# Kernel optimization log

Hardware: AMD Instinct MI355X
Metric: run time of the kernel (lower is better)

Reference implementation:

```python
import jax, jax.numpy as jnp
import numpy as np

N, E, G = 50000, 800000, 500
F_IN, H_DIM, L, NH, HD, OUT = 74, 256, 4, 8, 32, 1
SLOPE, EPS = 0.2, 1e-5


def setup_inputs() -> dict:
    key = jax.random.key(0)
    ks = jax.random.split(key, 24)
    rn = lambda k, s, sc: jax.random.normal(k, s, jnp.float32) * sc
    inp = {
        "x": jax.random.normal(ks[0], (N, F_IN), jnp.float32),
        "edge_index": jax.random.randint(ks[1], (2, E), 0, N),
        "batch": jnp.sort(jax.random.randint(ks[2], (N,), 0, G)),
        "in_w": rn(ks[3], (F_IN, H_DIM), 1.0 / np.sqrt(F_IN)),
        "in_b": jnp.zeros((H_DIM,), jnp.float32),
        "wl": rn(ks[4], (L, H_DIM, H_DIM), 1.0 / np.sqrt(H_DIM)),
        "wl_b": jnp.zeros((L, H_DIM), jnp.float32),
        "wr": rn(ks[5], (L, H_DIM, H_DIM), 1.0 / np.sqrt(H_DIM)),
        "wr_b": jnp.zeros((L, H_DIM), jnp.float32),
        "att": rn(ks[6], (L, NH, HD), 1.0 / np.sqrt(HD)),
        "gat_b": jnp.zeros((L, H_DIM), jnp.float32),
        "ln_g": jnp.ones((L, H_DIM), jnp.float32),
        "ln_b": jnp.zeros((L, H_DIM), jnp.float32),
        "out_w": rn(ks[7], (H_DIM, H_DIM), 1.0 / np.sqrt(H_DIM)),
        "out_b": jnp.zeros((H_DIM,), jnp.float32),
        "p1_w": rn(ks[8], (H_DIM, H_DIM // 2), 1.0 / np.sqrt(H_DIM)),
        "p1_b": jnp.zeros((H_DIM // 2,), jnp.float32),
        "bn1_g": jnp.ones((H_DIM // 2,), jnp.float32),
        "bn1_b": jnp.zeros((H_DIM // 2,), jnp.float32),
        "p2_w": rn(ks[9], (H_DIM // 2, H_DIM // 4), 1.0 / np.sqrt(H_DIM // 2)),
        "p2_b": jnp.zeros((H_DIM // 4,), jnp.float32),
        "bn2_g": jnp.ones((H_DIM // 4,), jnp.float32),
        "bn2_b": jnp.zeros((H_DIM // 4,), jnp.float32),
        "p3_w": rn(ks[10], (H_DIM // 4, OUT), 1.0 / np.sqrt(H_DIM // 4)),
        "p3_b": jnp.zeros((OUT,), jnp.float32),
    }
    return inp


def _layer_norm(x, g, b):
    m = x.mean(-1, keepdims=True)
    v = ((x - m) ** 2).mean(-1, keepdims=True)
    return (x - m) * jax.lax.rsqrt(v + EPS) * g + b


def _batch_norm(x, g, b):
    m = x.mean(0)
    v = ((x - m) ** 2).mean(0)
    return (x - m) * jax.lax.rsqrt(v + EPS) * g + b


def _gatv2(h, src, dst, wl, wl_b, wr, wr_b, att, bias, n):
    xl = (h @ wl + wl_b).reshape(n, NH, HD)  # source transform
    xr = (h @ wr + wr_b).reshape(n, NH, HD)  # target transform
    e = jax.nn.leaky_relu(xl[src] + xr[dst], SLOPE)      # [E, H, D]
    score = jnp.einsum('ehd,hd->eh', e, att)             # [E, H]
    smax = jax.ops.segment_max(score, dst, num_segments=n)
    num = jnp.exp(score - smax[dst])
    den = jax.ops.segment_sum(num, dst, num_segments=n)
    alpha = num / (den[dst] + 1e-16)                     # segment softmax per dst
    out = jax.ops.segment_sum(xl[src] * alpha[:, :, None], dst, num_segments=n)
    return out.reshape(n, NH * HD) + bias


def reference(x, edge_index, batch, in_w, in_b, wl, wl_b, wr, wr_b, att, gat_b,
              ln_g, ln_b, out_w, out_b, p1_w, p1_b, bn1_g, bn1_b,
              p2_w, p2_b, bn2_g, bn2_b, p3_w, p3_b):
    n = x.shape[0]
    loops = jnp.arange(n)
    src = jnp.concatenate([edge_index[0], loops])  # add self-loops (PyG default)
    dst = jnp.concatenate([edge_index[1], loops])
    h = x @ in_w + in_b
    for i in range(L):
        res = h
        g = _gatv2(h, src, dst, wl[i], wl_b[i], wr[i], wr_b[i], att[i], gat_b[i], n)
        if i > 0:
            g = g + res
        h = jax.nn.relu(_layer_norm(g, ln_g[i], ln_b[i]))
    h = h @ out_w + out_b
    cnt = jax.ops.segment_sum(jnp.ones((n,), h.dtype), batch, num_segments=G)
    gr = jax.ops.segment_sum(h, batch, num_segments=G) / jnp.maximum(cnt, 1.0)[:, None]
    z = jax.nn.relu(_batch_norm(gr @ p1_w + p1_b, bn1_g, bn1_b))
    z = jax.nn.relu(_batch_norm(z @ p2_w + p2_b, bn2_g, bn2_b))
    return z @ p3_w + p3_b
```

## Files before the change

kernel.cpp:

```cpp
#include <hip/hip_runtime.h>
#include <hip/hip_bf16.h>

#define F_IN   74
#define KPAD   96
#define HDIM   256
#define NHEAD  8
#define HEADD  32
#define NLAYER 4
#define SLOPE  0.2f
#define EPSN   1e-5f
#define LOG2E  1.44269504088896f

typedef __attribute__((ext_vector_type(8))) short bf16x8;
typedef __attribute__((ext_vector_type(4))) float f32x4;
typedef __attribute__((ext_vector_type(2))) float f32x2;

__device__ __forceinline__ float bf2f(unsigned short u){
  union { unsigned int i; float f; } x; x.i = ((unsigned int)u) << 16; return x.f;
}
__device__ __forceinline__ unsigned short f2bf(float f){
  union { float f; unsigned int i; } x; x.f = f;
  unsigned int u = x.i;
  return (unsigned short)((u + 0x7FFFu + ((u >> 16) & 1u)) >> 16);
}
__device__ __forceinline__ f32x2 bfpair(unsigned int u){
  union { unsigned int i; float f; } lo, hi;
  lo.i = u << 16; hi.i = u & 0xffff0000u;
  return (f32x2){lo.f, hi.f};
}
__device__ __forceinline__ float hw_exp2(float p){
  float r;
  asm volatile("v_exp_f32 %0, %1" : "=v"(r) : "v"(p));
  return r;
}
__device__ __forceinline__ float dpp_sum8(float p){
  int t;
  t = __builtin_amdgcn_update_dpp(0, __float_as_int(p), 0xB1, 0xF, 0xF, true);
  p += __int_as_float(t);
  t = __builtin_amdgcn_update_dpp(0, __float_as_int(p), 0x4E, 0xF, 0xF, true);
  p += __int_as_float(t);
  t = __builtin_amdgcn_update_dpp(0, __float_as_int(p), 0x141, 0xF, 0xF, true);
  p += __int_as_float(t);
  return p;
}
__device__ __forceinline__ float dpp_sum16(float p){
  int t;
  p = dpp_sum8(p);
  t = __builtin_amdgcn_update_dpp(0, __float_as_int(p), 0x140, 0xF, 0xF, true);
  p += __int_as_float(t);
  return p;
}

#define GLOAD16(g, s) __builtin_amdgcn_global_load_lds( \
  (const __attribute__((address_space(1))) void*)(g), \
  (__attribute__((address_space(3))) void*)(s), 16, 0, 0)

__global__ void k_hist(const int* __restrict__ dst, int* __restrict__ deg, int e){
  int i = blockIdx.x * 256 + threadIdx.x;
  if (i < e) atomicAdd(&deg[dst[i]], 1);
}

__global__ __launch_bounds__(256) void k_scan1(const int* __restrict__ deg,
    int* __restrict__ rowp, int* __restrict__ bsum, int n){
  __shared__ int wsum[4];
  const int tid = threadIdx.x, lane = tid & 63, wid = tid >> 6;
  const int i = blockIdx.x * 256 + tid;
  int v = (i < n) ? (deg[i] + 1) : 0;
  int xv = v;
  #pragma unroll
  for (int off = 1; off < 64; off <<= 1){
    int t = __shfl_up(xv, off);
    if (lane >= off) xv += t;
  }
  if (lane == 63) wsum[wid] = xv;
  __syncthreads();
  int woff = 0, total = 0;
  #pragma unroll
  for (int w = 0; w < 4; ++w){
    int s = wsum[w];
    total += s;
    if (w < wid) woff += s;
  }
  if (i < n) rowp[i] = woff + xv - v;
  if (tid == 0) bsum[blockIdx.x] = total;
}
__global__ __launch_bounds__(256) void k_scan2(const int* __restrict__ bsum,
    int* __restrict__ boff, int nb){
  __shared__ int wsum[4];
  const int tid = threadIdx.x, lane = tid & 63, wid = tid >> 6;
  int v = (tid < nb) ? bsum[tid] : 0;
  int xv = v;
  #pragma unroll
  for (int off = 1; off < 64; off <<= 1){
    int t = __shfl_up(xv, off);
    if (lane >= off) xv += t;
  }
  if (lane == 63) wsum[wid] = xv;
  __syncthreads();
  int woff = 0, total = 0;
  #pragma unroll
  for (int w = 0; w < 4; ++w){
    int s = wsum[w];
    total += s;
    if (w < wid) woff += s;
  }
  if (tid <= nb) boff[tid] = woff + xv - v;
  if (tid == 0) boff[nb] = total;
}
__global__ void k_scan3(int* __restrict__ rowp, int* __restrict__ cur,
                        const int* __restrict__ boff, int n, int nb){
  int i = blockIdx.x * 256 + threadIdx.x;
  if (i < n){
    int v = rowp[i] + boff[blockIdx.x];
    rowp[i] = v;
    cur[i] = v;
  }
  if (i == 0) rowp[n] = boff[nb];
}

__global__ void k_fill2(const int* __restrict__ src, const int* __restrict__ dst,
                        int* __restrict__ cur, unsigned int* __restrict__ csr,
                        int e, int n){
  int i = blockIdx.x * 256 + threadIdx.x;
  if (i < e){
    int p = atomicAdd(&cur[dst[i]], 1);
    csr[p] = ((unsigned int)src[i]) << 10;
  } else if (i < e + n){
    int v = i - e;
    int p = atomicAdd(&cur[v], 1);
    csr[p] = ((unsigned int)v) << 10;
  }
}

__global__ __launch_bounds__(256) void k_prep(
    const float* __restrict__ wl, const float* __restrict__ wr,
    const float* __restrict__ out_w, const float* __restrict__ in_w,
    const float* __restrict__ wl_b, const float* __restrict__ wr_b,
    const float* __restrict__ x,
    unsigned short* __restrict__ WtLR, unsigned short* __restrict__ WtO,
    unsigned short* __restrict__ WtI, float* __restrict__ bconc,
    unsigned short* __restrict__ xb, int n)
{
  const int b = blockIdx.x;
  const int tid = threadIdx.x;
  if (b < 576){
    __shared__ float tile[32][33];
    const float* Wm;
    unsigned short* Wo;
    int rem, colbase;
    if (b < 512){
      const int matset = b >> 8;
      const int mat = (b >> 6) & 3;
      rem = b & 63;
      const float* srcw = matset ? wr : wl;
      Wm = srcw + (size_t)mat * HDIM * HDIM;
      Wo = WtLR + (size_t)mat * 512 * HDIM;
      colbase = matset * 256;
    } else {
      rem = b - 512;
      Wm = out_w; Wo = WtO; colbase = 0;
    }
    const int c0 = (rem & 7) * 32, r0 = (rem >> 3) * 32;
    const int tx = tid & 31, ty = tid >> 5;
    #pragma unroll
    for (int i = 0; i < 32; i += 8)
      tile[ty + i][tx] = Wm[(size_t)(r0 + ty + i) * HDIM + c0 + tx];
    __syncthreads();
    #pragma unroll
    for (int i = 0; i < 32; i += 8){
      const int col = colbase + c0 + ty + i;
      const int k   = r0 + tx;
      const int cb = col >> 4, ks = k >> 5;
      const int lf = (col & 15) | (((k >> 3) & 3) << 4);
      Wo[((size_t)(cb * 8 + ks) * 64 + lf) * 8 + (k & 7)] = f2bf(tile[tx][ty + i]);
    }
  } else if (b < 672){
    int idx = (b - 576) * 256 + tid;
    int c = idx / KPAD, k = idx - c * KPAD;
    float v = (k < F_IN) ? in_w[(size_t)k * HDIM + c] : 0.f;
    WtI[idx] = f2bf(v);
  } else if (b < 680){
    int i = (b - 672) * 256 + tid;
    if (i < NLAYER * 512){
      int layer = i >> 9, c = i & 511;
      bconc[i] = (c < 256) ? wl_b[layer * 256 + c] : wr_b[layer * 256 + (c - 256)];
    }
  } else {
    int idx = (b - 680) * 256 + tid;
    if (idx < n * KPAD){
      int row = idx / KPAD, k = idx - row * KPAD;
      float v = (k < F_IN) ? x[(size_t)row * F_IN + k] : 0.f;
      xb[idx] = f2bf(v);
    }
  }
}

__global__ __launch_bounds__(256) void k_inproj_mfma(
    const unsigned short* __restrict__ xb, const unsigned short* __restrict__ Wt,
    const float* __restrict__ bias, unsigned short* __restrict__ C, int M)
{
  const int l = threadIdx.x & 63;
  const int w = threadIdx.x >> 6;
  const int wm = w >> 1, wn = w & 1;
  const int row0 = blockIdx.x * 128;
  const int col0 = blockIdx.y * 128;

  f32x4 acc[4][4];
  #pragma unroll
  for (int i = 0; i < 4; ++i)
    #pragma unroll
    for (int j = 0; j < 4; ++j) acc[i][j] = (f32x4){0.f, 0.f, 0.f, 0.f};

  #pragma unroll
  for (int kk = 0; kk < 3; ++kk){
    const int kof = kk * 32 + (l >> 4) * 8;
    bf16x8 af[4], bfr[4];
    #pragma unroll
    for (int mi = 0; mi < 4; ++mi){
      int row = row0 + wm * 64 + mi * 16 + (l & 15);
      if (row > M - 1) row = M - 1;
      af[mi] = *(const bf16x8*)(xb + (size_t)row * KPAD + kof);
    }
    #pragma unroll
    for (int ni = 0; ni < 4; ++ni){
      const int col = col0 + wn * 64 + ni * 16 + (l & 15);
      bfr[ni] = *(const bf16x8*)(Wt + (size_t)col * KPAD + kof);
    }
    #pragma unroll
    for (int mi = 0; mi < 4; ++mi)
      #pragma unroll
      for (int ni = 0; ni < 4; ++ni)
        acc[mi][ni] = __builtin_amdgcn_mfma_f32_16x16x32_bf16(
            af[mi], bfr[ni], acc[mi][ni], 0, 0, 0);
  }

  #pragma unroll
  for (int mi = 0; mi < 4; ++mi){
    #pragma unroll
    for (int ni = 0; ni < 4; ++ni){
      const int col = col0 + wn * 64 + ni * 16 + (l & 15);
      const float bv = bias[col];
      #pragma unroll
      for (int r = 0; r < 4; ++r){
        const int row = row0 + wm * 64 + mi * 16 + (l >> 4) * 4 + r;
        if (row < M) C[(size_t)row * HDIM + col] = f2bf(acc[mi][ni][r] + bv);
      }
    }
  }
}

__global__ __launch_bounds__(256) void k_gemm_mfma(
    const unsigned short* __restrict__ A, const unsigned short* __restrict__ Wt,
    const float* __restrict__ bias, unsigned short* __restrict__ C, int M, int ldc)
{
  __shared__ unsigned short As[2][128 * 64];
  const int tid = threadIdx.x;
  const int l   = tid & 63;
  const int w   = tid >> 6;
  const int wm  = w >> 1, wn = w & 1;
  const int row0 = blockIdx.x * 128;
  const int col0 = blockIdx.y * 128;

  const int srow   = l >> 3;
  const int schunk = l & 7;

  f32x4 acc[4][4];
  #pragma unroll
  for (int i = 0; i < 4; ++i)
    #pragma unroll
    for (int j = 0; j < 4; ++j) acc[i][j] = (f32x4){0.f, 0.f, 0.f, 0.f};

  auto stageA = [&](int buf, int k0){
    #pragma unroll
    for (int i = 0; i < 4; ++i){
      const int rloc = w * 32 + i * 8 + srow;
      const int sw   = (schunk ^ (rloc & 7)) * 16;
      int ra = row0 + rloc; if (ra > M - 1) ra = M - 1;
      const char* srcA = (const char*)(A + (size_t)ra * HDIM + k0) + sw;
      GLOAD16(srcA, &As[buf][(w * 32 + i * 8) * 64]);
    }
  };

  const unsigned short* Bf = Wt + ((size_t)(col0 / 16 + wn * 4) * 8 * 64 + l) * 8;

  stageA(0, 0);
  asm volatile("s_waitcnt vmcnt(0)" ::: "memory");
  __builtin_amdgcn_s_barrier();
  int buf = 0;
  #pragma unroll
  for (int t = 0; t < 4; ++t){
    bf16x8 bfr[2][4];
    #pragma unroll
    for (int kk = 0; kk < 2; ++kk)
      #pragma unroll
      for (int ni = 0; ni < 4; ++ni)
        bfr[kk][ni] = *(const bf16x8*)(Bf + ((size_t)ni * 8 + (t * 2 + kk)) * 64 * 8);
    if (t < 3) stageA(buf ^ 1, (t + 1) * 64);
    #pragma unroll
    for (int kk = 0; kk < 2; ++kk){
      bf16x8 af[4];
      #pragma unroll
      for (int mi = 0; mi < 4; ++mi){
        const int row = wm * 64 + mi * 16 + (l & 15);
        const int tt  = (kk * 4 + (l >> 4)) ^ (row & 7);
        af[mi] = *(const bf16x8*)((const char*)&As[buf][0] + row * 128 + tt * 16);
      }
      #pragma unroll
      for (int mi = 0; mi < 4; ++mi)
        #pragma unroll
        for (int ni = 0; ni < 4; ++ni)
          acc[mi][ni] = __builtin_amdgcn_mfma_f32_16x16x32_bf16(
              af[mi], bfr[kk][ni], acc[mi][ni], 0, 0, 0);
    }
    if (t < 3){
      asm volatile("s_waitcnt vmcnt(0)" ::: "memory");
      __builtin_amdgcn_s_barrier();
      buf ^= 1;
    }
  }

  #pragma unroll
  for (int mi = 0; mi < 4; ++mi){
    #pragma unroll
    for (int ni = 0; ni < 4; ++ni){
      const int col = col0 + wn * 64 + ni * 16 + (l & 15);
      const float bv = bias[col];
      #pragma unroll
      for (int r = 0; r < 4; ++r){
        const int row = row0 + wm * 64 + mi * 16 + (l >> 4) * 4 + r;
        if (row < M) C[(size_t)row * ldc + col] = f2bf(acc[mi][ni][r] + bv);
      }
    }
  }
}

__global__ __launch_bounds__(256) void k_gat(
    const unsigned short* __restrict__ xlr,
    const int* __restrict__ rp, const unsigned int* __restrict__ csr,
    const float* __restrict__ att, const float* __restrict__ gb,
    const float* __restrict__ lg, const float* __restrict__ lb,
    const unsigned short* __restrict__ hold, unsigned short* __restrict__ hnew,
    int n, int use_res)
{
  const int node = blockIdx.x * 4 + (threadIdx.x >> 6);
  if (node >= n) return;
  const int lane = threadIdx.x & 63;
  const int elem = lane << 2;
  const int head = lane >> 3;
  float4 attv = *(const float4*)(att + head * HEADD + (elem & 31));
  const f32x2 av01 = {attv.x * LOG2E, attv.y * LOG2E};
  const f32x2 av23 = {attv.z * LOG2E, attv.w * LOG2E};
  uint2 ur = *(const uint2*)(xlr + (size_t)node * 512 + 256 + elem);
  const f32x2 r01 = bfpair(ur.x), r23 = bfpair(ur.y);

  const unsigned int ebyte = (unsigned int)(elem << 1);
  const char* xb8 = (const char*)xlr;

  f32x2 a01 = {0.f, 0.f}, a23 = {0.f, 0.f};
  float l = 0.f;

  auto edgeq = [&](uint2 uu, f32x2& x01, f32x2& x23)->float{
    x01 = bfpair(uu.x); x23 = bfpair(uu.y);
    f32x2 t01 = x01 + r01, t23 = x23 + r23;
    f32x2 m01 = __builtin_elementwise_max(t01, t01 * SLOPE);
    f32x2 m23 = __builtin_elementwise_max(t23, t23 * SLOPE);
    f32x2 d = m01 * av01 + m23 * av23;
    float p = dpp_sum8(d.x + d.y);
    return hw_exp2(p);
  };

  const int e0 = rp[node], e1 = rp[node + 1];
  int e = e0;
  for (; e + 4 <= e1; e += 4){
    unsigned int o0 = csr[e] | ebyte, o1 = csr[e + 1] | ebyte;
    unsigned int o2 = csr[e + 2] | ebyte, o3 = csr[e + 3] | ebyte;
    uint2 u0 = *(const uint2*)(xb8 + o0);
    uint2 u1 = *(const uint2*)(xb8 + o1);
    uint2 u2 = *(const uint2*)(xb8 + o2);
    uint2 u3 = *(const uint2*)(xb8 + o3);
    f32x2 x01, x23;
    float q0 = edgeq(u0, x01, x23);
    a01 += q0 * x01; a23 += q0 * x23;
    float q1 = edgeq(u1, x01, x23);
    a01 += q1 * x01; a23 += q1 * x23;
    float q2 = edgeq(u2, x01, x23);
    a01 += q2 * x01; a23 += q2 * x23;
    float q3 = edgeq(u3, x01, x23);
    a01 += q3 * x01; a23 += q3 * x23;
    l += (q0 + q1) + (q2 + q3);
  }
  for (; e < e1; ++e){
    unsigned int o = csr[e] | ebyte;
    uint2 u = *(const uint2*)(xb8 + o);
    f32x2 x01, x23;
    float q = edgeq(u, x01, x23);
    l += q;
    a01 += q * x01; a23 += q * x23;
  }

  const float inv = 1.f / l;
  const size_t base = (size_t)node * HDIM + elem;
  float f0 = a01.x * inv + gb[elem + 0];
  float f1 = a01.y * inv + gb[elem + 1];
  float f2 = a23.x * inv + gb[elem + 2];
  float f3 = a23.y * inv + gb[elem + 3];
  if (use_res){
    ushort4 hv = *(const ushort4*)(hold + base);
    f0 += bf2f(hv.x); f1 += bf2f(hv.y); f2 += bf2f(hv.z); f3 += bf2f(hv.w);
  }
  float s = f0 + f1 + f2 + f3;
  s = dpp_sum16(s);
  s += __shfl_xor(s, 16);
  s += __shfl_xor(s, 32);
  const float mean = s * (1.f / HDIM);
  float d0 = f0 - mean, d1 = f1 - mean, d2 = f2 - mean, d3 = f3 - mean;
  float q = d0 * d0 + d1 * d1 + d2 * d2 + d3 * d3;
  q = dpp_sum16(q);
  q += __shfl_xor(q, 16);
  q += __shfl_xor(q, 32);
  const float rs = rsqrtf(q * (1.f / HDIM) + EPSN);
  float o0 = d0 * rs * lg[elem + 0] + lb[elem + 0]; o0 = o0 > 0.f ? o0 : 0.f;
  float o1 = d1 * rs * lg[elem + 1] + lb[elem + 1]; o1 = o1 > 0.f ? o1 : 0.f;
  float o2 = d2 * rs * lg[elem + 2] + lb[elem + 2]; o2 = o2 > 0.f ? o2 : 0.f;
  float o3 = d3 * rs * lg[elem + 3] + lb[elem + 3]; o3 = o3 > 0.f ? o3 : 0.f;
  ushort4 st; st.x = f2bf(o0); st.y = f2bf(o1); st.z = f2bf(o2); st.w = f2bf(o3);
  *(ushort4*)(hnew + base) = st;
}

__global__ __launch_bounds__(256) void k_pool2(
    const unsigned short* __restrict__ ho, const int* __restrict__ batch,
    float* __restrict__ gr, int n)
{
  const int g = blockIdx.x;
  int lo = 0, hi = n;
  while (lo < hi){ int mid = (lo + hi) >> 1; if (batch[mid] < g) lo = mid + 1; else hi = mid; }
  const int s = lo;
  hi = n;
  while (lo < hi){ int mid = (lo + hi) >> 1; if (batch[mid] < g + 1) lo = mid + 1; else hi = mid; }
  const int e = lo;
  const int j = threadIdx.x;
  float acc = 0.f;
  for (int i = s; i < e; ++i) acc += bf2f(ho[(size_t)i * HDIM + j]);
  int c = e - s; if (c < 1) c = 1;
  gr[(size_t)g * HDIM + j] = acc / (float)c;
}

__global__ void k_fc(const float* __restrict__ in, const float* __restrict__ w,
                     const float* __restrict__ b, float* __restrict__ out,
                     int kin, int kout){
  __shared__ float s[256];
  int g = blockIdx.x, j = threadIdx.x;
  for (int k = j; k < kin; k += blockDim.x) s[k] = in[(size_t)g * kin + k];
  __syncthreads();
  float a = b[j];
  for (int k = 0; k < kin; ++k) a = fmaf(s[k], w[k * kout + j], a);
  out[(size_t)g * kout + j] = a;
}

__global__ __launch_bounds__(256) void k_bn(float* __restrict__ z,
    const float* __restrict__ gam, const float* __restrict__ bet, int g_, int c_){
  const int c = blockIdx.x;
  float s = 0.f, s2 = 0.f;
  for (int r = threadIdx.x; r < g_; r += 256){
    float v = z[(size_t)r * c_ + c];
    s += v; s2 += v * v;
  }
  #pragma unroll
  for (int off = 1; off < 64; off <<= 1){ s += __shfl_xor(s, off); s2 += __shfl_xor(s2, off); }
  __shared__ float sw[4], sw2[4];
  __shared__ float smean, srstd;
  int lane = threadIdx.x & 63, wid = threadIdx.x >> 6;
  if (lane == 0){ sw[wid] = s; sw2[wid] = s2; }
  __syncthreads();
  if (threadIdx.x == 0){
    float ts = sw[0] + sw[1] + sw[2] + sw[3];
    float ts2 = sw2[0] + sw2[1] + sw2[2] + sw2[3];
    float mm = ts / g_;
    float vv = ts2 / g_ - mm * mm;
    smean = mm; srstd = rsqrtf(vv + EPSN);
  }
  __syncthreads();
  const float mm = smean, rs = srstd, gg = gam[c], bb = bet[c];
  for (int r = threadIdx.x; r < g_; r += 256){
    float v = (z[(size_t)r * c_ + c] - mm) * rs * gg + bb;
    z[(size_t)r * c_ + c] = v > 0.f ? v : 0.f;
  }
}

__global__ __launch_bounds__(256) void k_out(const float* __restrict__ z,
    const float* __restrict__ w, const float* __restrict__ b,
    float* __restrict__ out, int g_){
  int g = blockIdx.x * 4 + (threadIdx.x >> 6);
  if (g >= g_) return;
  int lane = threadIdx.x & 63;
  float v = z[(size_t)g * 64 + lane] * w[lane];
  #pragma unroll
  for (int off = 1; off < 64; off <<= 1) v += __shfl_xor(v, off);
  if (lane == 0) out[g] = v + b[0];
}

extern "C" void kernel_launch(void* const* d_in, const int* in_sizes, int n_in,
                              void* d_out, int out_size, void* d_ws, size_t ws_size,
                              hipStream_t stream)
{
  const float* x     = (const float*)d_in[0];
  const int*   ei    = (const int*)  d_in[1];
  const int*   batch = (const int*)  d_in[2];
  const float* in_w  = (const float*)d_in[3];
  const float* in_b  = (const float*)d_in[4];
  const float* wl    = (const float*)d_in[5];
  const float* wl_b  = (const float*)d_in[6];
  const float* wr    = (const float*)d_in[7];
  const float* wr_b  = (const float*)d_in[8];
  const float* att   = (const float*)d_in[9];
  const float* gat_b = (const float*)d_in[10];
  const float* ln_g  = (const float*)d_in[11];
  const float* ln_b  = (const float*)d_in[12];
  const float* out_w = (const float*)d_in[13];
  const float* out_b = (const float*)d_in[14];
  const float* p1_w  = (const float*)d_in[15];
  const float* p1_b  = (const float*)d_in[16];
  const float* bn1_g = (const float*)d_in[17];
  const float* bn1_b = (const float*)d_in[18];
  const float* p2_w  = (const float*)d_in[19];
  const float* p2_b  = (const float*)d_in[20];
  const float* bn2_g = (const float*)d_in[21];
  const float* bn2_b = (const float*)d_in[22];
  const float* p3_w  = (const float*)d_in[23];
  const float* p3_b  = (const float*)d_in[24];

  const int n = in_sizes[0] / F_IN;
  const int e = in_sizes[1] / 2;
  const int g = out_size;
  const int nb = (n + 255) / 256;

  char* p = (char*)d_ws;
  auto take = [&](size_t bytes)->char*{
    char* q = p; p += ((bytes + 255) & ~(size_t)255); return q;
  };
  unsigned short* hA   = (unsigned short*)take((size_t)n * HDIM * 2);
  unsigned short* hB   = (unsigned short*)take((size_t)n * HDIM * 2);
  unsigned short* xlr  = (unsigned short*)take((size_t)n * 512 * 2);
  unsigned short* WtLR = (unsigned short*)take((size_t)NLAYER * 512 * HDIM * 2);
  unsigned short* WtO  = (unsigned short*)take((size_t)HDIM * HDIM * 2);
  unsigned short* WtI  = (unsigned short*)take((size_t)HDIM * KPAD * 2);
  float* bconc = (float*)take((size_t)NLAYER * 512 * 4);
  int*   deg   = (int*)take((size_t)n * 4);
  int*   rowp  = (int*)take((size_t)(n + 1) * 4);
  int*   cur   = (int*)take((size_t)n * 4);
  unsigned int* csr = (unsigned int*)take((size_t)(e + n) * 4);
  int*   bsum  = (int*)take((size_t)(nb + 1) * 4);
  int*   boff  = (int*)take((size_t)(nb + 1) * 4);
  float* gr    = (float*)take((size_t)g * HDIM * 4);
  float* z1    = (float*)take((size_t)g * 128 * 4);
  float* z2    = (float*)take((size_t)g * 64 * 4);
  unsigned short* xb = xlr;
  (void)ws_size; (void)n_in;

  hipMemsetAsync(deg, 0, (size_t)n * 4, stream);
  k_hist<<<(e + 255) / 256, 256, 0, stream>>>(ei + e, deg, e);
  k_scan1<<<nb, 256, 0, stream>>>(deg, rowp, bsum, n);
  k_scan2<<<1, 256, 0, stream>>>(bsum, boff, nb);
  k_scan3<<<nb, 256, 0, stream>>>(rowp, cur, boff, n, nb);
  k_fill2<<<(e + n + 255) / 256, 256, 0, stream>>>(ei, ei + e, cur, csr, e, n);

  const int xconv_blocks = (n * KPAD + 255) / 256;
  k_prep<<<680 + xconv_blocks, 256, 0, stream>>>(
      wl, wr, out_w, in_w, wl_b, wr_b, x, WtLR, WtO, WtI, bconc, xb, n);

  k_inproj_mfma<<<dim3((n + 127) / 128, 2), 256, 0, stream>>>(xb, WtI, in_b, hA, n);

  unsigned short* hcur = hA;
  unsigned short* hnext = hB;
  for (int i = 0; i < NLAYER; ++i){
    k_gemm_mfma<<<dim3((n + 127) / 128, 4), 256, 0, stream>>>(
        hcur, WtLR + (size_t)i * 512 * HDIM, bconc + i * 512, xlr, n, 512);
    k_gat<<<(n + 3) / 4, 256, 0, stream>>>(xlr, rowp, csr,
        att + (size_t)i * NHEAD * HEADD, gat_b + i * HDIM,
        ln_g + i * HDIM, ln_b + i * HDIM, hcur, hnext, n, i > 0 ? 1 : 0);
    unsigned short* t = hcur; hcur = hnext; hnext = t;
  }
  k_gemm_mfma<<<dim3((n + 127) / 128, 2), 256, 0, stream>>>(
      hcur, WtO, out_b, hnext, n, HDIM);

  k_pool2<<<g, 256, 0, stream>>>(hnext, batch, gr, n);

  k_fc<<<g, 128, 0, stream>>>(gr, p1_w, p1_b, z1, HDIM, 128);
  k_bn<<<128, 256, 0, stream>>>(z1, bn1_g, bn1_b, g, 128);
  k_fc<<<g, 64, 0, stream>>>(z1, p2_w, p2_b, z2, 128, 64);
  k_bn<<<64, 256, 0, stream>>>(z2, bn2_g, bn2_b, g, 64);
  k_out<<<(g + 3) / 4, 256, 0, stream>>>(z2, p3_w, p3_b, (float*)d_out, g);
}
```

Before: 664.3 us.

## Split wave into two half-waves processing alternate edges with 16B gathers

```diff
diff --git a/kernel.cpp b/kernel.cpp
--- a/kernel.cpp
+++ b/kernel.cpp
@@ -33,19 +33,19 @@
   asm volatile("v_exp_f32 %0, %1" : "=v"(r) : "v"(p));
   return r;
 }
-__device__ __forceinline__ float dpp_sum8(float p){
+__device__ __forceinline__ float dpp_sum4(float p){
   int t;
   t = __builtin_amdgcn_update_dpp(0, __float_as_int(p), 0xB1, 0xF, 0xF, true);
   p += __int_as_float(t);
   t = __builtin_amdgcn_update_dpp(0, __float_as_int(p), 0x4E, 0xF, 0xF, true);
   p += __int_as_float(t);
+  return p;
+}
+__device__ __forceinline__ float dpp_sum16(float p){
+  int t;
+  p = dpp_sum4(p);
   t = __builtin_amdgcn_update_dpp(0, __float_as_int(p), 0x141, 0xF, 0xF, true);
   p += __int_as_float(t);
-  return p;
-}
-__device__ __forceinline__ float dpp_sum16(float p){
-  int t;
-  p = dpp_sum8(p);
   t = __builtin_amdgcn_update_dpp(0, __float_as_int(p), 0x140, 0xF, 0xF, true);
   p += __int_as_float(t);
   return p;
@@ -345,86 +345,112 @@
   const int node = blockIdx.x * 4 + (threadIdx.x >> 6);
   if (node >= n) return;
   const int lane = threadIdx.x & 63;
-  const int elem = lane << 2;
-  const int head = lane >> 3;
-  float4 attv = *(const float4*)(att + head * HEADD + (elem & 31));
-  const f32x2 av01 = {attv.x * LOG2E, attv.y * LOG2E};
-  const f32x2 av23 = {attv.z * LOG2E, attv.w * LOG2E};
-  uint2 ur = *(const uint2*)(xlr + (size_t)node * 512 + 256 + elem);
-  const f32x2 r01 = bfpair(ur.x), r23 = bfpair(ur.y);
-
-  const unsigned int ebyte = (unsigned int)(elem << 1);
+  const int sub  = lane & 31;
+  const int pair = lane >> 5;
+  const int ch0  = sub << 3;
+  const int head = sub >> 2;
+
+  float4 av_lo = *(const float4*)(att + head * HEADD + ((sub & 3) << 3));
+  float4 av_hi = *(const float4*)(att + head * HEADD + ((sub & 3) << 3) + 4);
+  const f32x2 av0 = {av_lo.x * LOG2E, av_lo.y * LOG2E};
+  const f32x2 av1 = {av_lo.z * LOG2E, av_lo.w * LOG2E};
+  const f32x2 av2 = {av_hi.x * LOG2E, av_hi.y * LOG2E};
+  const f32x2 av3 = {av_hi.z * LOG2E, av_hi.w * LOG2E};
+
+  uint4 ur = *(const uint4*)(xlr + (size_t)node * 512 + 256 + ch0);
+  const f32x2 r0 = bfpair(ur.x), r1 = bfpair(ur.y), r2 = bfpair(ur.z), r3 = bfpair(ur.w);
+
+  const unsigned int cbyte = (unsigned int)(ch0 << 1);
   const char* xb8 = (const char*)xlr;
 
-  f32x2 a01 = {0.f, 0.f}, a23 = {0.f, 0.f};
+  f32x2 a0 = {0.f,0.f}, a1 = {0.f,0.f}, a2 = {0.f,0.f}, a3 = {0.f,0.f};
   float l = 0.f;
 
-  auto edgeq = [&](uint2 uu, f32x2& x01, f32x2& x23)->float{
-    x01 = bfpair(uu.x); x23 = bfpair(uu.y);
-    f32x2 t01 = x01 + r01, t23 = x23 + r23;
-    f32x2 m01 = __builtin_elementwise_max(t01, t01 * SLOPE);
-    f32x2 m23 = __builtin_elementwise_max(t23, t23 * SLOPE);
-    f32x2 d = m01 * av01 + m23 * av23;
-    float p = dpp_sum8(d.x + d.y);
+  auto edgeq = [&](uint4 u, f32x2& x0, f32x2& x1, f32x2& x2, f32x2& x3)->float{
+    x0 = bfpair(u.x); x1 = bfpair(u.y); x2 = bfpair(u.z); x3 = bfpair(u.w);
+    f32x2 t0 = x0 + r0, t1 = x1 + r1, t2 = x2 + r2, t3 = x3 + r3;
+    f32x2 m0 = __builtin_elementwise_max(t0, t0 * SLOPE);
+    f32x2 m1 = __builtin_elementwise_max(t1, t1 * SLOPE);
+    f32x2 m2 = __builtin_elementwise_max(t2, t2 * SLOPE);
+    f32x2 m3 = __builtin_elementwise_max(t3, t3 * SLOPE);
+    f32x2 d = m0 * av0 + m1 * av1 + m2 * av2 + m3 * av3;
+    float p = dpp_sum4(d.x + d.y);
     return hw_exp2(p);
   };
 
   const int e0 = rp[node], e1 = rp[node + 1];
   int e = e0;
   for (; e + 4 <= e1; e += 4){
-    unsigned int o0 = csr[e] | ebyte, o1 = csr[e + 1] | ebyte;
-    unsigned int o2 = csr[e + 2] | ebyte, o3 = csr[e + 3] | ebyte;
-    uint2 u0 = *(const uint2*)(xb8 + o0);
-    uint2 u1 = *(const uint2*)(xb8 + o1);
-    uint2 u2 = *(const uint2*)(xb8 + o2);
-    uint2 u3 = *(const uint2*)(xb8 + o3);
-    f32x2 x01, x23;
-    float q0 = edgeq(u0, x01, x23);
-    a01 += q0 * x01; a23 += q0 * x23;
-    float q1 = edgeq(u1, x01, x23);
-    a01 += q1 * x01; a23 += q1 * x23;
-    float q2 = edgeq(u2, x01, x23);
-    a01 += q2 * x01; a23 += q2 * x23;
-    float q3 = edgeq(u3, x01, x23);
-    a01 += q3 * x01; a23 += q3 * x23;
-    l += (q0 + q1) + (q2 + q3);
-  }
-  for (; e < e1; ++e){
-    unsigned int o = csr[e] | ebyte;
-    uint2 u = *(const uint2*)(xb8 + o);
-    f32x2 x01, x23;
-    float q = edgeq(u, x01, x23);
+    unsigned int o0 = csr[e + pair] | cbyte;
+    unsigned int o1 = csr[e + 2 + pair] | cbyte;
+    uint4 u0 = *(const uint4*)(xb8 + o0);
+    uint4 u1 = *(const uint4*)(xb8 + o1);
+    f32x2 x0, x1, x2, x3;
+    float q0 = edgeq(u0, x0, x1, x2, x3);
+    a0 += q0 * x0; a1 += q0 * x1; a2 += q0 * x2; a3 += q0 * x3;
+    float q1 = edgeq(u1, x0, x1, x2, x3);
+    a0 += q1 * x0; a1 += q1 * x1; a2 += q1 * x2; a3 += q1 * x3;
+    l += q0 + q1;
+  }
+  for (; e < e1; e += 2){
+    int idx = e + pair;
+    unsigned int o = csr[(idx < e1) ? idx : (e1 - 1)] | cbyte;
+    uint4 u = *(const uint4*)(xb8 + o);
+    f32x2 x0, x1, x2, x3;
+    float q = edgeq(u, x0, x1, x2, x3);
+    q = (idx < e1) ? q : 0.f;
+    a0 += q * x0; a1 += q * x1; a2 += q * x2; a3 += q * x3;
     l += q;
-    a01 += q * x01; a23 += q * x23;
-  }
+  }
+
+  l    += __shfl_xor(l, 32);
+  a0.x += __shfl_xor(a0.x, 32); a0.y += __shfl_xor(a0.y, 32);
+  a1.x += __shfl_xor(a1.x, 32); a1.y += __shfl_xor(a1.y, 32);
+  a2.x += __shfl_xor(a2.x, 32); a2.y += __shfl_xor(a2.y, 32);
+  a3.x += __shfl_xor(a3.x, 32); a3.y += __shfl_xor(a3.y, 32);
 
   const float inv = 1.f / l;
-  const size_t base = (size_t)node * HDIM + elem;
-  float f0 = a01.x * inv + gb[elem + 0];
-  float f1 = a01.y * inv + gb[elem + 1];
-  float f2 = a23.x * inv + gb[elem + 2];
-  float f3 = a23.y * inv + gb[elem + 3];
+  float f[8];
+  f[0] = a0.x * inv; f[1] = a0.y * inv;
+  f[2] = a1.x * inv; f[3] = a1.y * inv;
+  f[4] = a2.x * inv; f[5] = a2.y * inv;
+  f[6] = a3.x * inv; f[7] = a3.y * inv;
+  {
+    float4 g_lo = *(const float4*)(gb + ch0);
+    float4 g_hi = *(const float4*)(gb + ch0 + 4);
+    f[0] += g_lo.x; f[1] += g_lo.y; f[2] += g_lo.z; f[3] += g_lo.w;
+    f[4] += g_hi.x; f[5] += g_hi.y; f[6] += g_hi.z; f[7] += g_hi.w;
+  }
   if (use_res){
-    ushort4 hv = *(const ushort4*)(hold + base);
-    f0 += bf2f(hv.x); f1 += bf2f(hv.y); f2 += bf2f(hv.z); f3 += bf2f(hv.w);
-  }
-  float s = f0 + f1 + f2 + f3;
+    uint4 hv = *(const uint4*)(hold + (size_t)node * HDIM + ch0);
+    f32x2 h0 = bfpair(hv.x), h1 = bfpair(hv.y), h2 = bfpair(hv.z), h3 = bfpair(hv.w);
+    f[0] += h0.x; f[1] += h0.y; f[2] += h1.x; f[3] += h1.y;
+    f[4] += h2.x; f[5] += h2.y; f[6] += h3.x; f[7] += h3.y;
+  }
+  float s = ((f[0] + f[1]) + (f[2] + f[3])) + ((f[4] + f[5]) + (f[6] + f[7]));
   s = dpp_sum16(s);
   s += __shfl_xor(s, 16);
-  s += __shfl_xor(s, 32);
   const float mean = s * (1.f / HDIM);
-  float d0 = f0 - mean, d1 = f1 - mean, d2 = f2 - mean, d3 = f3 - mean;
-  float q = d0 * d0 + d1 * d1 + d2 * d2 + d3 * d3;
-  q = dpp_sum16(q);
-  q += __shfl_xor(q, 16);
-  q += __shfl_xor(q, 32);
-  const float rs = rsqrtf(q * (1.f / HDIM) + EPSN);
-  float o0 = d0 * rs * lg[elem + 0] + lb[elem + 0]; o0 = o0 > 0.f ? o0 : 0.f;
-  float o1 = d1 * rs * lg[elem + 1] + lb[elem + 1]; o1 = o1 > 0.f ? o1 : 0.f;
-  float o2 = d2 * rs * lg[elem + 2] + lb[elem + 2]; o2 = o2 > 0.f ? o2 : 0.f;
-  float o3 = d3 * rs * lg[elem + 3] + lb[elem + 3]; o3 = o3 > 0.f ? o3 : 0.f;
-  ushort4 st; st.x = f2bf(o0); st.y = f2bf(o1); st.z = f2bf(o2); st.w = f2bf(o3);
-  *(ushort4*)(hnew + base) = st;
+  float d2 = 0.f;
+  float dd[8];
+  #pragma unroll
+  for (int j = 0; j < 8; ++j){ dd[j] = f[j] - mean; d2 += dd[j] * dd[j]; }
+  d2 = dpp_sum16(d2);
+  d2 += __shfl_xor(d2, 16);
+  const float rs = rsqrtf(d2 * (1.f / HDIM) + EPSN);
+  float4 lg_lo = *(const float4*)(lg + ch0), lg_hi = *(const float4*)(lg + ch0 + 4);
+  float4 lb_lo = *(const float4*)(lb + ch0), lb_hi = *(const float4*)(lb + ch0 + 4);
+  float og[8] = {lg_lo.x, lg_lo.y, lg_lo.z, lg_lo.w, lg_hi.x, lg_hi.y, lg_hi.z, lg_hi.w};
+  float ob[8] = {lb_lo.x, lb_lo.y, lb_lo.z, lb_lo.w, lb_hi.x, lb_hi.y, lb_hi.z, lb_hi.w};
+  bf16x8 st;
+  #pragma unroll
+  for (int j = 0; j < 8; ++j){
+    float v = dd[j] * rs * og[j] + ob[j];
+    v = v > 0.f ? v : 0.f;
+    st[j] = (short)f2bf(v);
+  }
+  if (pair == 0)
+    *(bf16x8*)(hnew + (size_t)node * HDIM + ch0) = st;
 }
 
 __global__ __launch_bounds__(256) void k_pool2(
```

After: 659.1 us. Within noise of the previous version (-0.8%).
